# Optimization experiments

Hardware: AMD Instinct MI355X
Metric: run time of the kernel (lower is better)

Reference implementation:

```python
import jax, jax.numpy as jnp
import numpy as np

BN_EPS = 1e-5


def conv1x1(x, w, b=None):
    # x: (B,Cin,F,T), w: (Cout,Cin)
    y = jnp.einsum('oc,bcft->boft', w, x)
    if b is not None:
        y = y + b[None, :, None, None]
    return y


def maxpool2(x):
    B, C, F, T = x.shape
    return x.reshape(B, C, F // 2, 2, T // 2, 2).max(axis=(3, 5))


def pos_grid(F, T, dtype):
    # flattened (F*T,) f-position and t-position in [0,1]
    fpos = jnp.linspace(0.0, 1.0, F, dtype=dtype)
    tpos = jnp.linspace(0.0, 1.0, T, dtype=dtype)
    fg = jnp.broadcast_to(fpos[:, None], (F, T)).reshape(-1)
    tg = jnp.broadcast_to(tpos[None, :], (F, T)).reshape(-1)
    return fg, tg


def setup_inputs() -> dict:
    key = jax.random.key(0)
    ks = jax.random.split(key, 12)
    B, C, F, T = 16, 64, 64, 64
    IC = 32  # inter_channels
    s = 0.05
    inp = {
        'x': jax.random.normal(ks[0], (B, C, F, T), jnp.float32),
        'psi_w': jax.random.normal(ks[1], (IC, C), jnp.float32) * s,
        'psi_b': jax.random.normal(ks[2], (IC,), jnp.float32) * s,
        'theta_w': jax.random.normal(ks[3], (IC, C), jnp.float32) * s,
        'theta_b': jax.random.normal(ks[4], (IC,), jnp.float32) * s,
        'phi_w': jax.random.normal(ks[5], (IC, C), jnp.float32) * s,
        'phi_b': jax.random.normal(ks[6], (IC,), jnp.float32) * s,
        'concat_w': jax.random.normal(ks[7], (2 * IC + 2,), jnp.float32) * s,  # 1x1 conv, no bias
        'W_w': jax.random.normal(ks[8], (C, IC + 1), jnp.float32) * s,
        'W_b': jax.random.normal(ks[9], (C,), jnp.float32) * s,
        'bn_gamma': jax.random.normal(ks[10], (C,), jnp.float32) * s + 1.0,
        'bn_beta': jax.random.normal(ks[11], (C,), jnp.float32) * s,
    }
    return inp


def reference(x, psi_w, psi_b, theta_w, theta_b, phi_w, phi_b, concat_w, W_w, W_b, bn_gamma, bn_beta):
    B, C, F, T = x.shape
    IC = psi_w.shape[0]
    # psi / phi are sub-sampled (maxpool 2x2) per sub_sample=True
    psi = maxpool2(conv1x1(x, psi_w, psi_b))            # (B,IC,F/2,T/2)
    theta = conv1x1(x, theta_w, theta_b)                # (B,IC,F,T)
    phi = maxpool2(conv1x1(x, phi_w, phi_b))            # (B,IC,F/2,T/2)

    h = F * T
    Fp, Tp = phi.shape[2], phi.shape[3]
    w = Fp * Tp

    psi_x = psi.reshape(B, IC, w).transpose(0, 2, 1)    # (B,w,IC)
    th_flat = theta.reshape(B, IC, h)                   # (B,IC,h)
    ph_flat = phi.reshape(B, IC, w)                     # (B,IC,w)

    # concat_project is a 1x1 conv over cat([theta, phi, pos_delta]) -> score separates:
    # f[b,i,j] = relu(w_th.theta_i + w_d.pos_i + w_ph.phi_j - w_d.pos_j)
    w_th = concat_w[:IC]
    w_ph = concat_w[IC:2 * IC]
    w_d = concat_w[2 * IC:]

    fg_q, tg_q = pos_grid(F, T, x.dtype)                # (h,)
    fg_k, tg_k = pos_grid(Fp, Tp, x.dtype)              # (w,)

    a = jnp.einsum('c,bcn->bn', w_th, th_flat) + (w_d[0] * fg_q + w_d[1] * tg_q)[None, :]  # (B,h)
    c = jnp.einsum('c,bcn->bn', w_ph, ph_flat) - (w_d[0] * fg_k + w_d[1] * tg_k)[None, :]  # (B,w)

    f = jax.nn.relu(a[:, :, None] + c[:, None, :])      # (B,h,w)
    f_div_C = f / jnp.asarray(w, x.dtype)
    # note: scaled_softmax(f) feeds only calc_relation_structure; with 'zero' the
    # structure feature is zeros, so the softmax does not affect the output.

    y = jnp.matmul(f_div_C, psi_x)                      # (B,h,IC)
    y = y.transpose(0, 2, 1).reshape(B, IC, F, T)
    structure_feat = jnp.zeros((B, 1, F, T), x.dtype)   # r_structure_type='zero'
    y = jnp.concatenate([y, structure_feat], axis=1)    # (B,IC+1,F,T)

    wy = conv1x1(y, W_w, W_b)                           # (B,C,F,T)
    # BatchNorm2d, training-mode batch statistics (torch default forward)
    mean = wy.mean(axis=(0, 2, 3), keepdims=True)
    var = wy.var(axis=(0, 2, 3), keepdims=True)
    wy = (wy - mean) / jnp.sqrt(var + BN_EPS)
    wy = wy * bn_gamma[None, :, None, None] + bn_beta[None, :, None, None]

    return wy + x
```

## Files before the change

kernel.cpp:

```cpp
#include <hip/hip_runtime.h>

#define BB 16
#define CC 64
#define ICC 32
#define NN 4096
#define MM 1024

typedef __attribute__((ext_vector_type(8))) short short8;
typedef __attribute__((ext_vector_type(4))) float f32x4;

static __device__ __forceinline__ unsigned cvt_pk_bf16(float lo, float hi) {
    unsigned d;
    asm("v_cvt_pk_bf16_f32 %0, %1, %2" : "=v"(d) : "v"(lo), "v"(hi));
    return d;
}
static __device__ __forceinline__ short8 as_s8(uint4 u) {
    union { uint4 a; short8 b; } t; t.a = u; return t.b;
}

__global__ void __launch_bounds__(256) k_pool(
        const float* __restrict__ x,
        const float* __restrict__ psi_w, const float* __restrict__ psi_b,
        const float* __restrict__ phi_w, const float* __restrict__ phi_b,
        const float* __restrict__ theta_w, const float* __restrict__ theta_b,
        const float* __restrict__ concat_w,
        unsigned* __restrict__ psi_pk, float* __restrict__ c_buf,
        float* __restrict__ a_buf, float* __restrict__ sumbuf) {
    __shared__ float pw[CC * ICC];
    __shared__ float fw[CC * ICC];
    __shared__ float vth[CC];
    __shared__ float xt[CC * 64];
    __shared__ float sconst;
    int tid = threadIdx.x;
    int b = blockIdx.x >> 6;
    int mtile = blockIdx.x & 63;
    int fp = mtile >> 1;
    int tpb = (mtile & 1) * 16;

    if (blockIdx.x == 0 && tid < 2 * CC) sumbuf[tid] = 0.f;
    for (int i = tid; i < CC * ICC; i += 256) {
        int ic = i >> 6, c = i & 63;
        pw[c * ICC + ic] = psi_w[i];
        fw[c * ICC + ic] = phi_w[i];
    }
    if (tid < CC) {
        float s = 0.f;
        for (int ic = 0; ic < ICC; ++ic) s += concat_w[ic] * theta_w[ic * CC + tid];
        vth[tid] = s;
    }
    if (tid == 255) {
        float s = 0.f;
        for (int ic = 0; ic < ICC; ++ic) s += concat_w[ic] * theta_b[ic];
        sconst = s;
    }
    const float* xb = x + (size_t)b * CC * NN;
    for (int i = tid; i < 1024; i += 256) {
        int c = i >> 4, row = (i >> 3) & 1, jj = i & 7;
        float4 v = *(const float4*)(xb + c * NN + (2 * fp + row) * 64 + 2 * tpb + jj * 4);
        *(float4*)&xt[c * 64 + row * 32 + jj * 4] = v;
    }
    __syncthreads();

    int ic = tid & 31;
    int mp = tid >> 5;
    float p00=0,p01=0,p02=0,p03=0, p10=0,p11=0,p12=0,p13=0;
    float q00=0,q01=0,q02=0,q03=0, q10=0,q11=0,q12=0,q13=0;
    for (int c = 0; c < CC; ++c) {
        float4 r0 = *(const float4*)&xt[c * 64 + mp * 4];
        float4 r1 = *(const float4*)&xt[c * 64 + 32 + mp * 4];
        float wp = pw[c * ICC + ic], wf = fw[c * ICC + ic];
        p00 += wp*r0.x; p01 += wp*r0.y; p02 += wp*r1.x; p03 += wp*r1.y;
        p10 += wp*r0.z; p11 += wp*r0.w; p12 += wp*r1.z; p13 += wp*r1.w;
        q00 += wf*r0.x; q01 += wf*r0.y; q02 += wf*r1.x; q03 += wf*r1.y;
        q10 += wf*r0.z; q11 += wf*r0.w; q12 += wf*r1.z; q13 += wf*r1.w;
    }
    float pb = psi_b[ic], fb = phi_b[ic];
    float psi0 = fmaxf(fmaxf(p00,p01),fmaxf(p02,p03)) + pb;
    float psi1 = fmaxf(fmaxf(p10,p11),fmaxf(p12,p13)) + pb;
    float phi0 = fmaxf(fmaxf(q00,q01),fmaxf(q02,q03)) + fb;
    float phi1 = fmaxf(fmaxf(q10,q11),fmaxf(q12,q13)) + fb;

    int m0 = mtile * 16 + 2 * mp;
    float wd0 = concat_w[2 * ICC], wd1 = concat_w[2 * ICC + 1];
    float wph = concat_w[ICC + ic];
    float v0 = wph * phi0, v1 = wph * phi1;
    for (int off = 16; off >= 1; off >>= 1) {
        v0 += __shfl_xor(v0, off, 32);
        v1 += __shfl_xor(v1, off, 32);
    }
    if (ic == 0) {
        int tp = tpb + 2 * mp;
        c_buf[b * MM + m0]     = v0 - (wd0 * (fp * (1.f/31.f)) + wd1 * (tp * (1.f/31.f)));
        c_buf[b * MM + m0 + 1] = v1 - (wd0 * (fp * (1.f/31.f)) + wd1 * ((tp + 1) * (1.f/31.f)));
    }
    int mpg = mtile * 8 + mp;
    int ks = mpg >> 4, kg = (mpg >> 2) & 3, cidx = mpg & 3;
    psi_pk[b * 16384 + ks * 512 + (ic >> 4) * 256 + kg * 64 + (ic & 15) * 4 + cidx]
        = cvt_pk_bf16(psi0, psi1);

    if (ic < 8) {
        int pix = mp * 8 + ic;
        int row = pix >> 5, colo = pix & 31;
        float sa = 0.f;
        #pragma unroll 8
        for (int c = 0; c < CC; ++c) sa += vth[c] * xt[c * 64 + row * 32 + colo];
        int f = 2 * fp + row, t = 2 * tpb + colo;
        a_buf[b * NN + f * 64 + t] = sa + sconst + wd0 * (f * (1.f/63.f)) + wd1 * (t * (1.f/63.f));
    }
}

static __device__ __forceinline__ void mfma_step(
        int ks, const float* c_lds, int hi4, float a0, float a1,
        uint4 bu0, uint4 bu1,
        f32x4& acc00, f32x4& acc01, f32x4& acc10, f32x4& acc11) {
    float4 c0 = *(const float4*)&c_lds[ks * 32 + hi4 * 8];
    float4 c1 = *(const float4*)&c_lds[ks * 32 + hi4 * 8 + 4];
    uint4 up;
    up.x = cvt_pk_bf16(fmaxf(a0 + c0.x, 0.f), fmaxf(a0 + c0.y, 0.f));
    up.y = cvt_pk_bf16(fmaxf(a0 + c0.z, 0.f), fmaxf(a0 + c0.w, 0.f));
    up.z = cvt_pk_bf16(fmaxf(a0 + c1.x, 0.f), fmaxf(a0 + c1.y, 0.f));
    up.w = cvt_pk_bf16(fmaxf(a0 + c1.z, 0.f), fmaxf(a0 + c1.w, 0.f));
    short8 ua0 = as_s8(up);
    up.x = cvt_pk_bf16(fmaxf(a1 + c0.x, 0.f), fmaxf(a1 + c0.y, 0.f));
    up.y = cvt_pk_bf16(fmaxf(a1 + c0.z, 0.f), fmaxf(a1 + c0.w, 0.f));
    up.z = cvt_pk_bf16(fmaxf(a1 + c1.x, 0.f), fmaxf(a1 + c1.y, 0.f));
    up.w = cvt_pk_bf16(fmaxf(a1 + c1.z, 0.f), fmaxf(a1 + c1.w, 0.f));
    short8 ua1 = as_s8(up);
    short8 vb0 = as_s8(bu0), vb1 = as_s8(bu1);
    acc00 = __builtin_amdgcn_mfma_f32_16x16x32_bf16(ua0, vb0, acc00, 0, 0, 0);
    acc01 = __builtin_amdgcn_mfma_f32_16x16x32_bf16(ua0, vb1, acc01, 0, 0, 0);
    acc10 = __builtin_amdgcn_mfma_f32_16x16x32_bf16(ua1, vb0, acc10, 0, 0, 0);
    acc11 = __builtin_amdgcn_mfma_f32_16x16x32_bf16(ua1, vb1, acc11, 0, 0, 0);
}

__global__ void __launch_bounds__(256) k_attn(
        const float* __restrict__ a_buf, const float* __restrict__ c_buf,
        const unsigned* __restrict__ psi_pk,
        const float* __restrict__ W_w, const float* __restrict__ W_b,
        float* __restrict__ wy) {
    __shared__ float c_lds[MM];
    __shared__ float W_lds[CC * ICC];
    __shared__ float Wb_lds[CC];
    __shared__ float yT[ICC * 130];
    int tid = threadIdx.x;
    int b = blockIdx.x >> 5;
    int ntile = blockIdx.x & 31;
    for (int i = tid; i < MM; i += 256) c_lds[i] = c_buf[b * MM + i];
    for (int i = tid; i < CC * ICC; i += 256) W_lds[i] = W_w[(i >> 5) * (ICC + 1) + (i & 31)];
    if (tid < CC) Wb_lds[tid] = W_b[tid];

    int w = tid >> 6, lane = tid & 63;
    int lo4 = lane & 15, hi4 = lane >> 4;
    const float* ab = a_buf + b * NN + ntile * 128 + w * 32;
    float a0 = ab[lo4], a1 = ab[16 + lo4];

    f32x4 acc00 = {0.f,0.f,0.f,0.f}, acc01 = {0.f,0.f,0.f,0.f};
    f32x4 acc10 = {0.f,0.f,0.f,0.f}, acc11 = {0.f,0.f,0.f,0.f};

    const uint4* pf4 = (const uint4*)psi_pk + (size_t)b * 4096;
    __syncthreads();

    uint4 p0a = pf4[lane],       p0b = pf4[64 + lane];
    uint4 p1a = pf4[128 + lane], p1b = pf4[192 + lane];
    for (int ks = 0; ks < 32; ks += 2) {
        uint4 n0a, n0b, n1a, n1b;
        bool more = (ks + 2 < 32);
        if (more) {
            n0a = pf4[(ks + 2) * 128 + lane]; n0b = pf4[(ks + 2) * 128 + 64 + lane];
            n1a = pf4[(ks + 3) * 128 + lane]; n1b = pf4[(ks + 3) * 128 + 64 + lane];
        }
        mfma_step(ks,     c_lds, hi4, a0, a1, p0a, p0b, acc00, acc01, acc10, acc11);
        mfma_step(ks + 1, c_lds, hi4, a0, a1, p1a, p1b, acc00, acc01, acc10, acc11);
        if (more) { p0a = n0a; p0b = n0b; p1a = n1a; p1b = n1b; }
    }

    const float inv = 1.0f / (float)MM;
    #pragma unroll
    for (int r = 0; r < 4; ++r) {
        yT[lo4 * 130 + w * 32 + hi4 * 4 + r]             = acc00[r] * inv;
        yT[(16 + lo4) * 130 + w * 32 + hi4 * 4 + r]      = acc01[r] * inv;
        yT[lo4 * 130 + w * 32 + 16 + hi4 * 4 + r]        = acc10[r] * inv;
        yT[(16 + lo4) * 130 + w * 32 + 16 + hi4 * 4 + r] = acc11[r] * inv;
    }
    __syncthreads();

    int p = tid & 127, oh = tid >> 7;
    float yv[ICC];
    #pragma unroll
    for (int icx = 0; icx < ICC; ++icx) yv[icx] = yT[icx * 130 + p];
    float* wyp = wy + (size_t)b * CC * NN + ntile * 128 + p;
    #pragma unroll 4
    for (int od = 0; od < 32; ++od) {
        int o = oh * 32 + od;
        float s = Wb_lds[o];
        const float* wrow = &W_lds[o * ICC];
        #pragma unroll
        for (int icx = 0; icx < ICC; ++icx) s += wrow[icx] * yv[icx];
        wyp[o * NN] = s;
    }
}

__global__ void k_stats2(const float* __restrict__ wy, float* __restrict__ sumbuf) {
    int o = blockIdx.x & 63, b = blockIdx.x >> 6;
    int tid = threadIdx.x;
    const float4* p = (const float4*)(wy + ((size_t)(b * CC + o)) * NN);
    float s = 0.f, s2 = 0.f;
    #pragma unroll
    for (int i = 0; i < 4; ++i) {
        float4 v = p[tid + i * 256];
        s += v.x + v.y + v.z + v.w;
        s2 += v.x * v.x + v.y * v.y + v.z * v.z + v.w * v.w;
    }
    for (int off = 32; off >= 1; off >>= 1) {
        s += __shfl_xor(s, off, 64);
        s2 += __shfl_xor(s2, off, 64);
    }
    __shared__ float ws1[4], ws2[4];
    int wv = tid >> 6;
    if ((tid & 63) == 0) { ws1[wv] = s; ws2[wv] = s2; }
    __syncthreads();
    if (tid == 0) {
        atomicAdd(&sumbuf[o], ws1[0] + ws1[1] + ws1[2] + ws1[3]);
        atomicAdd(&sumbuf[CC + o], ws2[0] + ws2[1] + ws2[2] + ws2[3]);
    }
}

__global__ void k_bn(const float* __restrict__ sumbuf, const float* __restrict__ bn_gamma,
                     const float* __restrict__ bn_beta, float* __restrict__ scale_shift) {
    int o = threadIdx.x;
    if (o < CC) {
        float nN = (float)(BB * NN);
        float mean = sumbuf[o] / nN;
        float var = sumbuf[CC + o] / nN - mean * mean;
        float sc = bn_gamma[o] * rsqrtf(var + 1e-5f);
        scale_shift[o] = sc;
        scale_shift[CC + o] = bn_beta[o] - mean * sc;
    }
}

__global__ void k_final(float* __restrict__ out, const float* __restrict__ x,
                        const float* __restrict__ scale_shift) {
    size_t i = (size_t)blockIdx.x * blockDim.x + threadIdx.x;
    size_t tot = (size_t)BB * CC * NN / 4;
    if (i < tot) {
        float4 w4 = ((const float4*)out)[i];
        float4 x4 = ((const float4*)x)[i];
        int o = (int)((i >> 10) & 63);
        float sc = scale_shift[o], sh = scale_shift[CC + o];
        float4 r;
        r.x = w4.x * sc + sh + x4.x;
        r.y = w4.y * sc + sh + x4.y;
        r.z = w4.z * sc + sh + x4.z;
        r.w = w4.w * sc + sh + x4.w;
        ((float4*)out)[i] = r;
    }
}

extern "C" void kernel_launch(void* const* d_in, const int* in_sizes, int n_in,
                              void* d_out, int out_size, void* d_ws, size_t ws_size,
                              hipStream_t stream) {
    const float* x        = (const float*)d_in[0];
    const float* psi_w    = (const float*)d_in[1];
    const float* psi_b    = (const float*)d_in[2];
    const float* theta_w  = (const float*)d_in[3];
    const float* theta_b  = (const float*)d_in[4];
    const float* phi_w    = (const float*)d_in[5];
    const float* phi_b    = (const float*)d_in[6];
    const float* concat_w = (const float*)d_in[7];
    const float* W_w      = (const float*)d_in[8];
    const float* W_b      = (const float*)d_in[9];
    const float* bn_gamma = (const float*)d_in[10];
    const float* bn_beta  = (const float*)d_in[11];

    float* ws = (float*)d_ws;
    float*    a_buf  = ws;
    float*    c_buf  = a_buf + BB * NN;
    unsigned* psi_pk = (unsigned*)(c_buf + BB * MM);
    float*    sumbuf = (float*)(psi_pk + BB * 16384);
    float*    sc_sh  = sumbuf + 128;
    float*    wy     = (float*)d_out;

    k_pool<<<BB * 64, 256, 0, stream>>>(x, psi_w, psi_b, phi_w, phi_b,
                                        theta_w, theta_b, concat_w,
                                        psi_pk, c_buf, a_buf, sumbuf);
    k_attn<<<BB * 32, 256, 0, stream>>>(a_buf, c_buf, psi_pk, W_w, W_b, wy);
    k_stats2<<<BB * CC, 256, 0, stream>>>(wy, sumbuf);
    k_bn<<<1, 64, 0, stream>>>(sumbuf, bn_gamma, bn_beta, sc_sh);
    k_final<<<(BB * CC * NN / 4 + 255) / 256, 256, 0, stream>>>(wy, x, sc_sh);
}
```

Measured before the change: 140.4 us.

## Store intermediate wy in bf16 workspace and fold BN scale computation into final kernel

The attention kernel now writes the pre-BN output wy as bf16 into a separate workspace buffer instead of fp32 into the output. The stats and final kernels read that bf16 buffer, which halves the intermediate traffic. The separate k_bn launch is removed: each k_final block computes its channel's scale and shift from sumbuf. This drops one launch and cuts memory traffic, at the cost of bf16 rounding in wy, which also affects the BN statistics.

Result: faster. 136.0 us (-3.1%).

```diff
diff --git a/kernel.cpp b/kernel.cpp
--- a/kernel.cpp
+++ b/kernel.cpp
@@ -16,6 +16,9 @@
 }
 static __device__ __forceinline__ short8 as_s8(uint4 u) {
     union { uint4 a; short8 b; } t; t.a = u; return t.b;
+}
+static __device__ __forceinline__ float bf16_to_f32(unsigned u) {
+    return __uint_as_float(u << 16);
 }
 
 __global__ void __launch_bounds__(256) k_pool(
@@ -137,7 +140,7 @@
         const float* __restrict__ a_buf, const float* __restrict__ c_buf,
         const unsigned* __restrict__ psi_pk,
         const float* __restrict__ W_w, const float* __restrict__ W_b,
-        float* __restrict__ wy) {
+        unsigned short* __restrict__ wy16) {
     __shared__ float c_lds[MM];
     __shared__ float W_lds[CC * ICC];
     __shared__ float Wb_lds[CC];
@@ -188,7 +191,7 @@
     float yv[ICC];
     #pragma unroll
     for (int icx = 0; icx < ICC; ++icx) yv[icx] = yT[icx * 130 + p];
-    float* wyp = wy + (size_t)b * CC * NN + ntile * 128 + p;
+    unsigned short* wyp = wy16 + (size_t)b * CC * NN + ntile * 128 + p;
     #pragma unroll 4
     for (int od = 0; od < 32; ++od) {
         int o = oh * 32 + od;
@@ -196,20 +199,22 @@
         const float* wrow = &W_lds[o * ICC];
         #pragma unroll
         for (int icx = 0; icx < ICC; ++icx) s += wrow[icx] * yv[icx];
-        wyp[o * NN] = s;
-    }
-}
-
-__global__ void k_stats2(const float* __restrict__ wy, float* __restrict__ sumbuf) {
+        wyp[(size_t)o * NN] = (unsigned short)(cvt_pk_bf16(s, 0.f) & 0xffffu);
+    }
+}
+
+__global__ void k_stats2(const unsigned short* __restrict__ wy16, float* __restrict__ sumbuf) {
     int o = blockIdx.x & 63, b = blockIdx.x >> 6;
     int tid = threadIdx.x;
-    const float4* p = (const float4*)(wy + ((size_t)(b * CC + o)) * NN);
+    const uint2* p = (const uint2*)(wy16 + ((size_t)(b * CC + o)) * NN);
     float s = 0.f, s2 = 0.f;
     #pragma unroll
     for (int i = 0; i < 4; ++i) {
-        float4 v = p[tid + i * 256];
-        s += v.x + v.y + v.z + v.w;
-        s2 += v.x * v.x + v.y * v.y + v.z * v.z + v.w * v.w;
+        uint2 v = p[tid + i * 256];
+        float f0 = bf16_to_f32(v.x & 0xffffu), f1 = bf16_to_f32(v.x >> 16);
+        float f2 = bf16_to_f32(v.y & 0xffffu), f3 = bf16_to_f32(v.y >> 16);
+        s  += f0 + f1 + f2 + f3;
+        s2 += f0*f0 + f1*f1 + f2*f2 + f3*f3;
     }
     for (int off = 32; off >= 1; off >>= 1) {
         s += __shfl_xor(s, off, 64);
@@ -225,35 +230,32 @@
     }
 }
 
-__global__ void k_bn(const float* __restrict__ sumbuf, const float* __restrict__ bn_gamma,
-                     const float* __restrict__ bn_beta, float* __restrict__ scale_shift) {
-    int o = threadIdx.x;
-    if (o < CC) {
+__global__ void __launch_bounds__(256) k_final(
+        float* __restrict__ out, const float* __restrict__ x,
+        const unsigned short* __restrict__ wy16,
+        const float* __restrict__ sumbuf,
+        const float* __restrict__ bn_gamma, const float* __restrict__ bn_beta) {
+    __shared__ float s_sc, s_sh;
+    size_t i = (size_t)blockIdx.x * 256 + threadIdx.x;
+    int o = (int)((i >> 10) & 63);
+    if (threadIdx.x == 0) {
         float nN = (float)(BB * NN);
         float mean = sumbuf[o] / nN;
         float var = sumbuf[CC + o] / nN - mean * mean;
         float sc = bn_gamma[o] * rsqrtf(var + 1e-5f);
-        scale_shift[o] = sc;
-        scale_shift[CC + o] = bn_beta[o] - mean * sc;
-    }
-}
-
-__global__ void k_final(float* __restrict__ out, const float* __restrict__ x,
-                        const float* __restrict__ scale_shift) {
-    size_t i = (size_t)blockIdx.x * blockDim.x + threadIdx.x;
-    size_t tot = (size_t)BB * CC * NN / 4;
-    if (i < tot) {
-        float4 w4 = ((const float4*)out)[i];
-        float4 x4 = ((const float4*)x)[i];
-        int o = (int)((i >> 10) & 63);
-        float sc = scale_shift[o], sh = scale_shift[CC + o];
-        float4 r;
-        r.x = w4.x * sc + sh + x4.x;
-        r.y = w4.y * sc + sh + x4.y;
-        r.z = w4.z * sc + sh + x4.z;
-        r.w = w4.w * sc + sh + x4.w;
-        ((float4*)out)[i] = r;
-    }
+        s_sc = sc;
+        s_sh = bn_beta[o] - mean * sc;
+    }
+    __syncthreads();
+    float sc = s_sc, sh = s_sh;
+    uint2 wv = ((const uint2*)wy16)[i];
+    float4 x4 = ((const float4*)x)[i];
+    float4 r;
+    r.x = bf16_to_f32(wv.x & 0xffffu) * sc + sh + x4.x;
+    r.y = bf16_to_f32(wv.x >> 16)     * sc + sh + x4.y;
+    r.z = bf16_to_f32(wv.y & 0xffffu) * sc + sh + x4.z;
+    r.w = bf16_to_f32(wv.y >> 16)     * sc + sh + x4.w;
+    ((float4*)out)[i] = r;
 }
 
 extern "C" void kernel_launch(void* const* d_in, const int* in_sizes, int n_in,
@@ -273,18 +275,17 @@
     const float* bn_beta  = (const float*)d_in[11];
 
     float* ws = (float*)d_ws;
-    float*    a_buf  = ws;
-    float*    c_buf  = a_buf + BB * NN;
-    unsigned* psi_pk = (unsigned*)(c_buf + BB * MM);
-    float*    sumbuf = (float*)(psi_pk + BB * 16384);
-    float*    sc_sh  = sumbuf + 128;
-    float*    wy     = (float*)d_out;
+    float*          a_buf  = ws;
+    float*          c_buf  = a_buf + BB * NN;
+    unsigned*       psi_pk = (unsigned*)(c_buf + BB * MM);
+    float*          sumbuf = (float*)(psi_pk + BB * 16384);
+    unsigned short* wy16   = (unsigned short*)(ws + 344320);
+    float*          out    = (float*)d_out;
 
     k_pool<<<BB * 64, 256, 0, stream>>>(x, psi_w, psi_b, phi_w, phi_b,
                                         theta_w, theta_b, concat_w,
                                         psi_pk, c_buf, a_buf, sumbuf);
-    k_attn<<<BB * 32, 256, 0, stream>>>(a_buf, c_buf, psi_pk, W_w, W_b, wy);
-    k_stats2<<<BB * CC, 256, 0, stream>>>(wy, sumbuf);
-    k_bn<<<1, 64, 0, stream>>>(sumbuf, bn_gamma, bn_beta, sc_sh);
-    k_final<<<(BB * CC * NN / 4 + 255) / 256, 256, 0, stream>>>(wy, x, sc_sh);
-}
+    k_attn<<<BB * 32, 256, 0, stream>>>(a_buf, c_buf, psi_pk, W_w, W_b, wy16);
+    k_stats2<<<BB * CC, 256, 0, stream>>>(wy16, sumbuf);
+    k_final<<<BB * CC * NN / 1024, 256, 0, stream>>>(out, x, wy16, sumbuf, bn_gamma, bn_beta);
+}
```
